# Optimization experiments

Hardware: AMD Instinct MI355X
Metric: run time of the kernel (lower is better)

The kernel has to match this reference:

```python
import jax, jax.numpy as jnp
import numpy as np

BATCH, NODES, CH_IN, CH_OUT, N_EXPERTS = 8, 8192, 128, 128, 64

def setup_inputs() -> dict:
    key = jax.random.key(0)
    kx, kw, ks = jax.random.split(key, 3)
    x = jax.random.normal(kx, (BATCH, NODES, CH_IN), dtype=jnp.float32)
    # std = fan_in**-0.5 per self_init
    W = jax.random.normal(kw, (N_EXPERTS, CH_OUT, CH_IN), dtype=jnp.float32) * (CH_IN ** -0.5)
    sel = jax.random.randint(ks, (NODES,), 0, N_EXPERTS, dtype=jnp.int64)
    return {"x": x, "sel": sel, "W": W}

def reference(x, sel, W):
    # x: (b, n, j), W[sel]: (n, i, j) -> out: (b, n, i)
    Wsel = W[sel]  # gather a (ch_out, ch_in) matrix per node
    return jnp.einsum('bnj,nij->bni', x, Wsel)
```

## Files before the change

kernel.cpp:

```cpp
#include <hip/hip_runtime.h>
#include <hip/hip_bf16.h>

#define BATCH   8
#define NODES   8192
#define CH      128
#define NEXP    64
#define TN      16
#define MAXP    (NODES + NEXP * TN)
#define NTILES  (MAXP / TN)

typedef __attribute__((ext_vector_type(8))) short bf16x8;
typedef __attribute__((ext_vector_type(4))) float f32x4;

__device__ __forceinline__ short f2bf(float f) {
    union { float f; unsigned u; } v; v.f = f;
    unsigned r = (v.u + 0x7fffu + ((v.u >> 16) & 1u)) >> 16;
    return (short)r;
}

__device__ __forceinline__ bf16x8 cvt8(f32x4 lo, f32x4 hi) {
    bf16x8 r;
    r[0] = f2bf(lo[0]); r[1] = f2bf(lo[1]); r[2] = f2bf(lo[2]); r[3] = f2bf(lo[3]);
    r[4] = f2bf(hi[0]); r[5] = f2bf(hi[1]); r[6] = f2bf(hi[2]); r[7] = f2bf(hi[3]);
    return r;
}

__global__ __launch_bounds__(256)
void prep_kernel(const int* __restrict__ sel, const float* __restrict__ W,
                 short* __restrict__ Wbf, int* __restrict__ sorted)
{
    const int e = blockIdx.x;
    const int t = threadIdx.x;

    {
        const float* ws = W   + (size_t)e * CH * CH;
        short*       wd = Wbf + (size_t)e * CH * CH;
        #pragma unroll
        for (int i = 0; i < 8; ++i) {
            int idx = (i * 256 + t) * 8;
            f32x4 lo = *reinterpret_cast<const f32x4*>(ws + idx);
            f32x4 hi = *reinterpret_cast<const f32x4*>(ws + idx + 4);
            *reinterpret_cast<bf16x8*>(wd + idx) = cvt8(lo, hi);
        }
    }

    __shared__ int cnt[NEXP];
    __shared__ int s_off, s_cnt, cursor;
    if (t < NEXP) cnt[t] = 0;
    if (t == 0) cursor = 0;
    __syncthreads();

    int myv[NODES / 256];
    #pragma unroll
    for (int i = 0; i < NODES / 256; ++i) {
        myv[i] = sel[i * 256 + t];
        atomicAdd(&cnt[myv[i]], 1);
    }
    __syncthreads();

    if (t == 0) {
        int off = 0, myoff = 0;
        for (int ee = 0; ee < NEXP; ++ee) {
            if (ee == e) myoff = off;
            off += (cnt[ee] + TN - 1) & ~(TN - 1);
        }
        s_off = myoff;
        s_cnt = cnt[e];
    }
    __syncthreads();

    const int off = s_off, myc = s_cnt;
    const int pad = (myc + TN - 1) & ~(TN - 1);

    for (int i = myc + t; i < pad; i += 256) sorted[off + i] = -1;

    if (e == NEXP - 1) {
        for (int i = off + pad + t; i < MAXP; i += 256) sorted[i] = -1;
    }

    #pragma unroll
    for (int i = 0; i < NODES / 256; ++i) {
        if (myv[i] == e) {
            int pos = atomicAdd(&cursor, 1);
            sorted[off + pos] = i * 256 + t;
        }
    }
}

__global__ __launch_bounds__(256)
void gemm_kernel(const float* __restrict__ x, const int* __restrict__ sel,
                 const short* __restrict__ Wbf, float* __restrict__ out,
                 const int* __restrict__ sorted)
{
    __shared__ int s_nodes[TN];
    __shared__ int s_expert;

    const int tid  = threadIdx.x;
    const int tile = blockIdx.x;

    if (tid < TN) s_nodes[tid] = sorted[tile * TN + tid];
    if (tid == 0) {
        int n0 = sorted[tile * TN];
        s_expert = (n0 >= 0) ? sel[n0] : -1;
    }
    __syncthreads();

    const int e = s_expert;
    if (e < 0) return;

    const int wave = tid >> 6;
    const int lane = tid & 63;
    const int m16  = lane & 15;
    const int quad = lane >> 4;

    const float* xrow[2];
    #pragma unroll
    for (int rt = 0; rt < 2; ++rt) {
        int r    = wave * 32 + rt * 16 + m16;
        int node = s_nodes[r >> 3];
        int b    = r & 7;
        int nd   = (node >= 0) ? node : 0;
        xrow[rt] = x + ((size_t)(b * NODES + nd)) * CH;
    }
    const short* wbase = Wbf + (size_t)e * CH * CH;

    f32x4 acc[2][8];
    #pragma unroll
    for (int rt = 0; rt < 2; ++rt)
        #pragma unroll
        for (int ct = 0; ct < 8; ++ct)
            acc[rt][ct] = (f32x4){0.f, 0.f, 0.f, 0.f};

    #pragma unroll
    for (int kk = 0; kk < 4; ++kk) {
        const int k0 = kk * 32 + quad * 8;

        bf16x8 afrag[2];
        #pragma unroll
        for (int rt = 0; rt < 2; ++rt) {
            const float* p = xrow[rt] + k0;
            f32x4 lo = *reinterpret_cast<const f32x4*>(p);
            f32x4 hi = *reinterpret_cast<const f32x4*>(p + 4);
            afrag[rt] = cvt8(lo, hi);
        }

        #pragma unroll
        for (int ct = 0; ct < 8; ++ct) {
            bf16x8 bfrag = *reinterpret_cast<const bf16x8*>(
                wbase + (size_t)(ct * 16 + m16) * CH + k0);
            acc[0][ct] = __builtin_amdgcn_mfma_f32_16x16x32_bf16(
                             afrag[0], bfrag, acc[0][ct], 0, 0, 0);
            acc[1][ct] = __builtin_amdgcn_mfma_f32_16x16x32_bf16(
                             afrag[1], bfrag, acc[1][ct], 0, 0, 0);
        }
    }

    #pragma unroll
    for (int rt = 0; rt < 2; ++rt) {
        #pragma unroll
        for (int reg = 0; reg < 4; ++reg) {
            int r    = wave * 32 + rt * 16 + quad * 4 + reg;
            int node = s_nodes[r >> 3];
            if (node < 0) continue;
            int b = r & 7;
            float* orow = out + ((size_t)(b * NODES + node)) * CH;
            #pragma unroll
            for (int ct = 0; ct < 8; ++ct)
                orow[ct * 16 + m16] = acc[rt][ct][reg];
        }
    }
}

extern "C" void kernel_launch(void* const* d_in, const int* in_sizes, int n_in,
                              void* d_out, int out_size, void* d_ws, size_t ws_size,
                              hipStream_t stream)
{
    const float* x   = (const float*)d_in[0];
    const int*   sel = (const int*)  d_in[1];
    const float* W   = (const float*)d_in[2];
    float*       out = (float*)d_out;

    short* Wbf   = (short*)d_ws;
    int*   sorted = (int*)((char*)d_ws + (size_t)NEXP * CH * CH * sizeof(short));

    prep_kernel<<<NEXP, 256, 0, stream>>>(sel, W, Wbf, sorted);
    gemm_kernel<<<NTILES, 256, 0, stream>>>(x, sel, Wbf, out, sorted);
}
```

Before: 115.5 us.

## Split GEMM tiles into half-blocks, precompute tile experts, use nontemporal memory ops

The GEMM grid now launches two 128-thread blocks per 16-node tile, each handling 8 nodes. Half-blocks whose nodes are all padding exit early, and there are more, smaller blocks to spread the latency-bound work. The prep kernel replaces the serial per-expert offset loop with a wave-level prefix scan and writes a per-tile expert table, so GEMM blocks no longer read through sel. Streaming loads of x and W and stores of out use nontemporal hints to reduce cache pollution. In exchange, each half-block re-reads the expert weights from L2, which doubles weight traffic per tile.

```diff
diff --git a/kernel.cpp b/kernel.cpp
--- a/kernel.cpp
+++ b/kernel.cpp
@@ -27,7 +27,8 @@
 
 __global__ __launch_bounds__(256)
 void prep_kernel(const int* __restrict__ sel, const float* __restrict__ W,
-                 short* __restrict__ Wbf, int* __restrict__ sorted)
+                 short* __restrict__ Wbf, int* __restrict__ sorted,
+                 int* __restrict__ texp)
 {
     const int e = blockIdx.x;
     const int t = threadIdx.x;
@@ -38,8 +39,8 @@
         #pragma unroll
         for (int i = 0; i < 8; ++i) {
             int idx = (i * 256 + t) * 8;
-            f32x4 lo = *reinterpret_cast<const f32x4*>(ws + idx);
-            f32x4 hi = *reinterpret_cast<const f32x4*>(ws + idx + 4);
+            f32x4 lo = __builtin_nontemporal_load(reinterpret_cast<const f32x4*>(ws + idx));
+            f32x4 hi = __builtin_nontemporal_load(reinterpret_cast<const f32x4*>(ws + idx + 4));
             *reinterpret_cast<bf16x8*>(wd + idx) = cvt8(lo, hi);
         }
     }
@@ -58,14 +59,16 @@
     }
     __syncthreads();
 
-    if (t == 0) {
-        int off = 0, myoff = 0;
-        for (int ee = 0; ee < NEXP; ++ee) {
-            if (ee == e) myoff = off;
-            off += (cnt[ee] + TN - 1) & ~(TN - 1);
+    if (t < NEXP) {
+        int c = cnt[t];
+        int p = (c + TN - 1) & ~(TN - 1);
+        int s = p;
+        #pragma unroll
+        for (int d = 1; d < NEXP; d <<= 1) {
+            int o = __shfl_up(s, d, 64);
+            if (t >= d) s += o;
         }
-        s_off = myoff;
-        s_cnt = cnt[e];
+        if (t == e) { s_off = s - p; s_cnt = c; }
     }
     __syncthreads();
 
@@ -73,9 +76,9 @@
     const int pad = (myc + TN - 1) & ~(TN - 1);
 
     for (int i = myc + t; i < pad; i += 256) sorted[off + i] = -1;
-
+    for (int i = off / TN + t; i < (off + pad) / TN; i += 256) texp[i] = e;
     if (e == NEXP - 1) {
-        for (int i = off + pad + t; i < MAXP; i += 256) sorted[i] = -1;
+        for (int i = (off + pad) / TN + t; i < NTILES; i += 256) texp[i] = -1;
     }
 
     #pragma unroll
@@ -87,26 +90,25 @@
     }
 }
 
-__global__ __launch_bounds__(256)
-void gemm_kernel(const float* __restrict__ x, const int* __restrict__ sel,
-                 const short* __restrict__ Wbf, float* __restrict__ out,
-                 const int* __restrict__ sorted)
+__global__ __launch_bounds__(128)
+void gemm_kernel(const float* __restrict__ x, const short* __restrict__ Wbf,
+                 float* __restrict__ out, const int* __restrict__ sorted,
+                 const int* __restrict__ texp)
 {
-    __shared__ int s_nodes[TN];
-    __shared__ int s_expert;
+    __shared__ int s_nodes[8];
+    __shared__ int s_e;
 
     const int tid  = threadIdx.x;
-    const int tile = blockIdx.x;
+    const int tile = blockIdx.x >> 1;
+    const int half = blockIdx.x & 1;
 
-    if (tid < TN) s_nodes[tid] = sorted[tile * TN + tid];
-    if (tid == 0) {
-        int n0 = sorted[tile * TN];
-        s_expert = (n0 >= 0) ? sel[n0] : -1;
-    }
+    if (tid < 8) s_nodes[tid] = sorted[tile * TN + half * 8 + tid];
+    if (tid == 0) s_e = texp[tile];
     __syncthreads();
 
-    const int e = s_expert;
+    const int e = s_e;
     if (e < 0) return;
+    if (s_nodes[0] < 0) return;
 
     const int wave = tid >> 6;
     const int lane = tid & 63;
@@ -138,9 +140,9 @@
         bf16x8 afrag[2];
         #pragma unroll
         for (int rt = 0; rt < 2; ++rt) {
-            const float* p = xrow[rt] + k0;
-            f32x4 lo = *reinterpret_cast<const f32x4*>(p);
-            f32x4 hi = *reinterpret_cast<const f32x4*>(p + 4);
+            const f32x4* p = reinterpret_cast<const f32x4*>(xrow[rt] + k0);
+            f32x4 lo = __builtin_nontemporal_load(p);
+            f32x4 hi = __builtin_nontemporal_load(p + 1);
             afrag[rt] = cvt8(lo, hi);
         }
 
@@ -166,7 +168,7 @@
             float* orow = out + ((size_t)(b * NODES + node)) * CH;
             #pragma unroll
             for (int ct = 0; ct < 8; ++ct)
-                orow[ct * 16 + m16] = acc[rt][ct][reg];
+                __builtin_nontemporal_store(acc[rt][ct][reg], orow + ct * 16 + m16);
         }
     }
 }
@@ -180,9 +182,10 @@
     const float* W   = (const float*)d_in[2];
     float*       out = (float*)d_out;
 
-    short* Wbf   = (short*)d_ws;
+    short* Wbf    = (short*)d_ws;
     int*   sorted = (int*)((char*)d_ws + (size_t)NEXP * CH * CH * sizeof(short));
+    int*   texp   = sorted + MAXP;
 
-    prep_kernel<<<NEXP, 256, 0, stream>>>(sel, W, Wbf, sorted);
-    gemm_kernel<<<NTILES, 256, 0, stream>>>(x, sel, Wbf, out, sorted);
+    prep_kernel<<<NEXP, 256, 0, stream>>>(sel, W, Wbf, sorted, texp);
+    gemm_kernel<<<NTILES * 2, 128, 0, stream>>>(x, Wbf, out, sorted, texp);
 }
```

After: 119.7 us. 1.04x slower.
